# Optimization experiments

Measured on AMD Instinct MI355X. Metric: run time of the kernel, lower is better.

Reference implementation:

```python
import jax, jax.numpy as jnp
import numpy as np

DIM = 1024
HEADS = 16
HEAD_DIM = DIM // HEADS
MAX_SEQ = 4096
BATCH = 16
POSITION = MAX_SEQ - 1


def setup_inputs() -> dict:
    key = jax.random.key(0)
    ks = jax.random.split(key, 8)
    s = 0.02  # weight init scale, typical for transformer linears
    return {
        "token": jax.random.normal(ks[0], (BATCH, 1, DIM), dtype=jnp.float32),
        "k_cache": jax.random.normal(ks[1], (BATCH, MAX_SEQ, HEADS, HEAD_DIM), dtype=jnp.float32),
        "v_cache": jax.random.normal(ks[2], (BATCH, MAX_SEQ, HEADS, HEAD_DIM), dtype=jnp.float32),
        "Wq": jax.random.normal(ks[3], (DIM, DIM), dtype=jnp.float32) * s,
        "Wk": jax.random.normal(ks[4], (DIM, DIM), dtype=jnp.float32) * s,
        "Wv": jax.random.normal(ks[5], (DIM, DIM), dtype=jnp.float32) * s,
        "Wo": jax.random.normal(ks[6], (DIM, DIM), dtype=jnp.float32) * s,
        "position": POSITION,
    }


def reference(token, k_cache, v_cache, Wq, Wk, Wv, Wo, position):
    # Decode step: single-query attention against KV cache (FlexDecodingModule.decode).
    B = token.shape[0]
    # QKV projections (torch Linear: x @ W.T), bias=False
    q = (token @ Wq.T).reshape(B, 1, HEADS, HEAD_DIM)
    k = (token @ Wk.T).reshape(B, 1, HEADS, HEAD_DIM)
    v = (token @ Wv.T).reshape(B, 1, HEADS, HEAD_DIM)
    # Inline KV-cache append at `position` (static python int)
    kc = k_cache.at[:, position].set(k[:, 0])
    vc = v_cache.at[:, position].set(v[:, 0])
    past_k = kc[:, : position + 1]  # [B, L, H, D]
    past_v = vc[:, : position + 1]
    # Causal score_mod with offset=position, q_idx=0 => all kv_idx<=position visible (no mask)
    scale = 1.0 / np.sqrt(HEAD_DIM).astype(np.float32)
    scores = jnp.einsum("bqhd,bkhd->bhqk", q, past_k) * scale  # [B, H, 1, L]
    attn = jax.nn.softmax(scores, axis=-1)
    out = jnp.einsum("bhqk,bkhd->bqhd", attn, past_v)  # [B, 1, H, D]
    out = out.reshape(B, 1, DIM)
    return out @ Wo.T
```

## Files before the change

### kernel.cpp

```cpp
#include <hip/hip_runtime.h>
#include <hip/hip_bf16.h>
#include <math.h>

#define DIM 1024
#define HEADS 16
#define HEAD_DIM 64
#define MAXSEQ 4096
#define BATCH 16
#define SEQ_PER_BLK 32
#define NBLK (MAXSEQ / SEQ_PER_BLK)
#define NTILES (SEQ_PER_BLK / 4)

typedef float v4f __attribute__((ext_vector_type(4)));

__device__ __forceinline__ void gl16(v4f& dst, const float* p) {
  asm volatile("global_load_dwordx4 %0, %1, off" : "=v"(dst) : "v"(p)
               : "memory");
}

#define TILE_WAIT8(K, V)                                                     \
  asm volatile("s_waitcnt vmcnt(8)"                                          \
               : "+v"(K[0]), "+v"(K[1]), "+v"(K[2]), "+v"(K[3]),             \
                 "+v"(V[0]), "+v"(V[1]), "+v"(V[2]), "+v"(V[3])::"memory")
#define TILE_WAIT0(K, V)                                                     \
  asm volatile("s_waitcnt vmcnt(0)"                                          \
               : "+v"(K[0]), "+v"(K[1]), "+v"(K[2]), "+v"(K[3]),             \
                 "+v"(V[0]), "+v"(V[1]), "+v"(V[2]), "+v"(V[3])::"memory")

__global__ __launch_bounds__(256) void qkv_proj(
    const float* __restrict__ token,
    const float* __restrict__ Wq, const float* __restrict__ Wk,
    const float* __restrict__ Wv,
    float* __restrict__ out ) {
  __shared__ float tok[BATCH * DIM];
  for (int idx = threadIdx.x; idx < BATCH * DIM; idx += 256)
    tok[idx] = token[idx];
  __syncthreads();

  const float* W = (blockIdx.y == 0) ? Wq : ((blockIdx.y == 1) ? Wk : Wv);
  float* o = out + (size_t)blockIdx.y * BATCH * DIM;

  const int wave = threadIdx.x >> 6;
  const int lane = threadIdx.x & 63;
  const int i0 = blockIdx.x * 16 + wave * 4;

  float acc[4][16];
#pragma unroll
  for (int ii = 0; ii < 4; ++ii)
#pragma unroll
    for (int b = 0; b < 16; ++b) acc[ii][b] = 0.f;

  for (int t = 0; t < 16; ++t) {
    const int j = t * 64 + lane;
    float tk[16];
#pragma unroll
    for (int b = 0; b < 16; ++b) tk[b] = tok[b * DIM + j];
#pragma unroll
    for (int ii = 0; ii < 4; ++ii) {
      const float w = W[(size_t)(i0 + ii) * DIM + j];
#pragma unroll
      for (int b = 0; b < 16; ++b) acc[ii][b] = fmaf(w, tk[b], acc[ii][b]);
    }
  }

#pragma unroll
  for (int ii = 0; ii < 4; ++ii)
#pragma unroll
    for (int b = 0; b < 16; ++b) {
      float v = acc[ii][b];
#pragma unroll
      for (int m = 32; m >= 1; m >>= 1) v += __shfl_xor(v, m);
      if (lane == 0) o[(size_t)b * DIM + i0 + ii] = v;
    }
}

__global__ __launch_bounds__(256, 4) void attn_partial(
    const float* __restrict__ kc, const float* __restrict__ vc,
    const float* __restrict__ qkv, const int* __restrict__ pos_p,
    float* __restrict__ part) {
  const int blk = blockIdx.x, b = blockIdx.y;
  const int t = threadIdx.x;
  const int h = t >> 4, lq = t & 15;
  const int pos = pos_p[0];
  const int s0 = blk * SEQ_PER_BLK;

  const float scale = 0.125f;
  v4f q4 = *(const v4f*)(qkv + (size_t)b * DIM + 4 * t);
  q4 *= scale;
  __builtin_amdgcn_sched_barrier(0);

  const float* kp = kc + (size_t)b * MAXSEQ * DIM + (size_t)s0 * DIM + 4 * t;
  const float* vp = vc + (size_t)b * MAXSEQ * DIM + (size_t)s0 * DIM + 4 * t;

  v4f kb[2][4], vb[2][4];

  auto stage = [&](int buf) {
#pragma unroll
    for (int r = 0; r < 4; ++r) {
      gl16(kb[buf][r], kp); kp += DIM;
      gl16(vb[buf][r], vp); vp += DIM;
    }
  };

  float m = -INFINITY, lsum = 0.f;
  v4f a4 = {0.f, 0.f, 0.f, 0.f};

  auto compute = [&](int buf, int srow) {
    float sc[4];
#pragma unroll
    for (int r = 0; r < 4; ++r) {
      const v4f k4 = kb[buf][r];
      sc[r] = q4.x * k4.x + q4.y * k4.y + q4.z * k4.z + q4.w * k4.w;
    }
#pragma unroll
    for (int r = 0; r < 4; ++r) {
      sc[r] += __shfl_xor(sc[r], 1);
      sc[r] += __shfl_xor(sc[r], 2);
      sc[r] += __shfl_xor(sc[r], 4);
      sc[r] += __shfl_xor(sc[r], 8);
    }
#pragma unroll
    for (int r = 0; r < 4; ++r)
      if (srow + r >= pos) sc[r] = -INFINITY;

    const float tm = fmaxf(fmaxf(sc[0], sc[1]), fmaxf(sc[2], sc[3]));
    const float m_new = fmaxf(m, tm);
    const float corr = (m_new == -INFINITY) ? 1.f : __expf(m - m_new);
    lsum *= corr;
    a4 *= corr;
    m = m_new;
#pragma unroll
    for (int r = 0; r < 4; ++r) {
      const float pp = (sc[r] == -INFINITY) ? 0.f : __expf(sc[r] - m);
      lsum += pp;
      a4 += vb[buf][r] * pp;
    }
  };

  stage(0);
#pragma unroll
  for (int tt = 0; tt < NTILES - 1; ++tt) {
    stage((tt + 1) & 1);
    TILE_WAIT8(kb[tt & 1], vb[tt & 1]);
    __builtin_amdgcn_sched_barrier(0);
    compute(tt & 1, s0 + tt * 4);
  }
  TILE_WAIT0(kb[(NTILES - 1) & 1], vb[(NTILES - 1) & 1]);
  __builtin_amdgcn_sched_barrier(0);
  compute((NTILES - 1) & 1, s0 + (NTILES - 1) * 4);

  const size_t base = (((size_t)(b * HEADS + h)) * NBLK + blk) * 66;
  part[base + 2 + lq * 4 + 0] = a4.x;
  part[base + 2 + lq * 4 + 1] = a4.y;
  part[base + 2 + lq * 4 + 2] = a4.z;
  part[base + 2 + lq * 4 + 3] = a4.w;
  if (lq == 0) { part[base] = m; part[base + 1] = lsum; }
}

__global__ __launch_bounds__(256) void attn_combine(
    const float* __restrict__ part, const float* __restrict__ qkv,
    float* __restrict__ attn) {
  const int bh = blockIdx.x;
  const int b = bh >> 4, hh = bh & 15;
  const int g = threadIdx.x >> 6, d = threadIdx.x & 63;
  const float* p0 = part + (size_t)bh * NBLK * 66;

  const float qd = qkv[(size_t)b * DIM + hh * HEAD_DIM + d];
  const float kd = qkv[(size_t)BATCH * DIM + (size_t)b * DIM + hh * HEAD_DIM + d];
  const float vd = qkv[2 * (size_t)BATCH * DIM + (size_t)b * DIM + hh * HEAD_DIM + d];

  float sn = qd * kd;
  sn += __shfl_xor(sn, 1);
  sn += __shfl_xor(sn, 2);
  sn += __shfl_xor(sn, 4);
  sn += __shfl_xor(sn, 8);
  sn += __shfl_xor(sn, 16);
  sn += __shfl_xor(sn, 32);
  sn *= 0.125f;

  float M = sn;
  for (int c = g; c < NBLK; c += 4) M = fmaxf(M, p0[c * 66]);

  __shared__ float sM[4], sL[4], sO[4][64];
  if (d == 0) sM[g] = M;
  __syncthreads();
  M = fmaxf(fmaxf(sM[0], sM[1]), fmaxf(sM[2], sM[3]));

  float L = 0.f, o = 0.f;
  if (g == 0) {
    const float wn = __expf(sn - M);
    L = wn;
    o = wn * vd;
  }
  for (int c = g; c < NBLK; c += 4) {
    const float mc = p0[c * 66];
    if (mc > -INFINITY) {
      const float w = __expf(mc - M);
      L += p0[c * 66 + 1] * w;
      o = fmaf(p0[c * 66 + 2 + d], w, o);
    }
  }
  sO[g][d] = o;
  if (d == 0) sL[g] = L;
  __syncthreads();
  if (g == 0) {
    o = sO[0][d] + sO[1][d] + sO[2][d] + sO[3][d];
    L = sL[0] + sL[1] + sL[2] + sL[3];
    attn[(size_t)b * DIM + hh * HEAD_DIM + d] = o / L;
  }
}

__global__ __launch_bounds__(256) void o_proj(
    const float* __restrict__ attn, const float* __restrict__ Wo,
    float* __restrict__ out) {
  __shared__ float tok[BATCH * DIM];
  for (int idx = threadIdx.x; idx < BATCH * DIM; idx += 256)
    tok[idx] = attn[idx];
  __syncthreads();

  const int wave = threadIdx.x >> 6;
  const int lane = threadIdx.x & 63;
  const int i0 = blockIdx.x * 16 + wave * 4;

  float acc[4][16];
#pragma unroll
  for (int ii = 0; ii < 4; ++ii)
#pragma unroll
    for (int b = 0; b < 16; ++b) acc[ii][b] = 0.f;

  for (int t = 0; t < 16; ++t) {
    const int j = t * 64 + lane;
    float tk[16];
#pragma unroll
    for (int b = 0; b < 16; ++b) tk[b] = tok[b * DIM + j];
#pragma unroll
    for (int ii = 0; ii < 4; ++ii) {
      const float w = Wo[(size_t)(i0 + ii) * DIM + j];
#pragma unroll
      for (int b = 0; b < 16; ++b) acc[ii][b] = fmaf(w, tk[b], acc[ii][b]);
    }
  }

#pragma unroll
  for (int ii = 0; ii < 4; ++ii)
#pragma unroll
    for (int b = 0; b < 16; ++b) {
      float v = acc[ii][b];
#pragma unroll
      for (int m = 32; m >= 1; m >>= 1) v += __shfl_xor(v, m);
      if (lane == 0) out[(size_t)b * DIM + i0 + ii] = v;
    }
}

extern "C" void kernel_launch(void* const* d_in, const int* in_sizes, int n_in,
                              void* d_out, int out_size, void* d_ws, size_t ws_size,
                              hipStream_t stream) {
  const float* token = (const float*)d_in[0];
  const float* kc = (const float*)d_in[1];
  const float* vc = (const float*)d_in[2];
  const float* Wq = (const float*)d_in[3];
  const float* Wk = (const float*)d_in[4];
  const float* Wv = (const float*)d_in[5];
  const float* Wo = (const float*)d_in[6];
  const int* pos = (const int*)d_in[7];
  float* out = (float*)d_out;
  float* ws = (float*)d_ws;

  float* qkv = ws;
  float* part = ws + 3 * BATCH * DIM;
  float* attn = part + (size_t)BATCH * HEADS * NBLK * 66;

  hipLaunchKernelGGL(qkv_proj, dim3(64, 3), dim3(256), 0, stream,
                     token, Wq, Wk, Wv, qkv);
  hipLaunchKernelGGL(attn_partial, dim3(NBLK, BATCH), dim3(256), 0,
                     stream, kc, vc, qkv, pos, part);
  hipLaunchKernelGGL(attn_combine, dim3(BATCH * HEADS), dim3(256), 0, stream,
                     part, qkv, attn);
  hipLaunchKernelGGL(o_proj, dim3(64), dim3(256), 0, stream, attn, Wo, out);
  (void)in_sizes; (void)n_in; (void)out_size; (void)ws_size;
}
```

Baseline: 198.2 us.

## Remap attention partial so each wave streams full rows over its own sequence range

Reorganizes attn_partial so each wave owns a contiguous chunk of sequence rows and loads a whole 4KB row per step, with each lane holding four heads. Previously the 256 threads of a block split one row. Blocks drop from 128 to 32 per batch and each block yields four wave-level partials, so the combine kernel now reduces 128 partials per head. The change aims to lengthen per-wave streaming runs, cut the grid count and keep two rows in flight per wave. In exchange it uses more registers (occupancy hint lowered from 4 to 2 blocks) and launches fewer total blocks, which can reduce how many loads are outstanding at once across the GPU.

```diff
diff --git a/kernel.cpp b/kernel.cpp
--- a/kernel.cpp
+++ b/kernel.cpp
@@ -7,9 +7,10 @@
 #define HEAD_DIM 64
 #define MAXSEQ 4096
 #define BATCH 16
-#define SEQ_PER_BLK 32
-#define NBLK (MAXSEQ / SEQ_PER_BLK)
-#define NTILES (SEQ_PER_BLK / 4)
+#define NBLKS 32
+#define ROWS_PER_BLK (MAXSEQ / NBLKS)
+#define ROWS_PER_WAVE (ROWS_PER_BLK / 4)
+#define NPART (NBLKS * 4)
 
 typedef float v4f __attribute__((ext_vector_type(4)));
 
@@ -18,11 +19,11 @@
                : "memory");
 }
 
-#define TILE_WAIT8(K, V)                                                     \
+#define ROW_WAIT8(K, V)                                                      \
   asm volatile("s_waitcnt vmcnt(8)"                                          \
                : "+v"(K[0]), "+v"(K[1]), "+v"(K[2]), "+v"(K[3]),             \
                  "+v"(V[0]), "+v"(V[1]), "+v"(V[2]), "+v"(V[3])::"memory")
-#define TILE_WAIT0(K, V)                                                     \
+#define ROW_WAIT0(K, V)                                                      \
   asm volatile("s_waitcnt vmcnt(0)"                                          \
                : "+v"(K[0]), "+v"(K[1]), "+v"(K[2]), "+v"(K[3]),             \
                  "+v"(V[0]), "+v"(V[1]), "+v"(V[2]), "+v"(V[3])::"memory")
@@ -74,87 +75,111 @@
     }
 }
 
-__global__ __launch_bounds__(256, 4) void attn_partial(
+__global__ __launch_bounds__(256, 2) void attn_partial(
     const float* __restrict__ kc, const float* __restrict__ vc,
     const float* __restrict__ qkv, const int* __restrict__ pos_p,
     float* __restrict__ part) {
   const int blk = blockIdx.x, b = blockIdx.y;
   const int t = threadIdx.x;
-  const int h = t >> 4, lq = t & 15;
+  const int w = t >> 6, lane = t & 63;
+  const int g = lane >> 4, lq = lane & 15;
   const int pos = pos_p[0];
-  const int s0 = blk * SEQ_PER_BLK;
+  const int srow0 = blk * ROWS_PER_BLK + w * ROWS_PER_WAVE;
 
   const float scale = 0.125f;
-  v4f q4 = *(const v4f*)(qkv + (size_t)b * DIM + 4 * t);
-  q4 *= scale;
+  v4f q4[4];
+#pragma unroll
+  for (int i = 0; i < 4; ++i) {
+    q4[i] = *(const v4f*)(qkv + (size_t)b * DIM + (4 * i + g) * HEAD_DIM +
+                          lq * 4);
+    q4[i] *= scale;
+  }
   __builtin_amdgcn_sched_barrier(0);
 
-  const float* kp = kc + (size_t)b * MAXSEQ * DIM + (size_t)s0 * DIM + 4 * t;
-  const float* vp = vc + (size_t)b * MAXSEQ * DIM + (size_t)s0 * DIM + 4 * t;
-
-  v4f kb[2][4], vb[2][4];
-
-  auto stage = [&](int buf) {
-#pragma unroll
-    for (int r = 0; r < 4; ++r) {
-      gl16(kb[buf][r], kp); kp += DIM;
-      gl16(vb[buf][r], vp); vp += DIM;
+  const float* kp = kc + (size_t)b * MAXSEQ * DIM + (size_t)srow0 * DIM +
+                    lane * 4;
+  const float* vp = vc + (size_t)b * MAXSEQ * DIM + (size_t)srow0 * DIM +
+                    lane * 4;
+
+  v4f k0[4], v0[4], k1[4], v1[4];
+
+#define STAGE(K, V, r)                                                       \
+  {                                                                          \
+    const float* kr = kp + (size_t)(r)*DIM;                                  \
+    const float* vr = vp + (size_t)(r)*DIM;                                  \
+    gl16(K[0], kr); gl16(K[1], kr + 256);                                    \
+    gl16(K[2], kr + 512); gl16(K[3], kr + 768);                              \
+    gl16(V[0], vr); gl16(V[1], vr + 256);                                    \
+    gl16(V[2], vr + 512); gl16(V[3], vr + 768);                              \
+  }
+
+  float m[4], lsum[4];
+  v4f acc[4];
+#pragma unroll
+  for (int i = 0; i < 4; ++i) {
+    m[i] = -INFINITY;
+    lsum[i] = 0.f;
+    acc[i] = (v4f){0.f, 0.f, 0.f, 0.f};
+  }
+
+  auto compute = [&](const v4f (&K)[4], const v4f (&V)[4], int r) {
+    const int s = srow0 + r;
+    if (s >= pos) return;
+    float sc[4];
+#pragma unroll
+    for (int i = 0; i < 4; ++i)
+      sc[i] = q4[i].x * K[i].x + q4[i].y * K[i].y + q4[i].z * K[i].z +
+              q4[i].w * K[i].w;
+#pragma unroll
+    for (int i = 0; i < 4; ++i) {
+      sc[i] += __shfl_xor(sc[i], 1);
+      sc[i] += __shfl_xor(sc[i], 2);
+      sc[i] += __shfl_xor(sc[i], 4);
+      sc[i] += __shfl_xor(sc[i], 8);
+    }
+#pragma unroll
+    for (int i = 0; i < 4; ++i) {
+      const float mn = fmaxf(m[i], sc[i]);
+      const float corr = __expf(m[i] - mn);
+      const float p = __expf(sc[i] - mn);
+      lsum[i] = lsum[i] * corr + p;
+      acc[i] = acc[i] * corr + V[i] * p;
+      m[i] = mn;
     }
   };
 
-  float m = -INFINITY, lsum = 0.f;
-  v4f a4 = {0.f, 0.f, 0.f, 0.f};
-
-  auto compute = [&](int buf, int srow) {
-    float sc[4];
-#pragma unroll
-    for (int r = 0; r < 4; ++r) {
-      const v4f k4 = kb[buf][r];
-      sc[r] = q4.x * k4.x + q4.y * k4.y + q4.z * k4.z + q4.w * k4.w;
-    }
-#pragma unroll
-    for (int r = 0; r < 4; ++r) {
-      sc[r] += __shfl_xor(sc[r], 1);
-      sc[r] += __shfl_xor(sc[r], 2);
-      sc[r] += __shfl_xor(sc[r], 4);
-      sc[r] += __shfl_xor(sc[r], 8);
-    }
-#pragma unroll
-    for (int r = 0; r < 4; ++r)
-      if (srow + r >= pos) sc[r] = -INFINITY;
-
-    const float tm = fmaxf(fmaxf(sc[0], sc[1]), fmaxf(sc[2], sc[3]));
-    const float m_new = fmaxf(m, tm);
-    const float corr = (m_new == -INFINITY) ? 1.f : __expf(m - m_new);
-    lsum *= corr;
-    a4 *= corr;
-    m = m_new;
-#pragma unroll
-    for (int r = 0; r < 4; ++r) {
-      const float pp = (sc[r] == -INFINITY) ? 0.f : __expf(sc[r] - m);
-      lsum += pp;
-      a4 += vb[buf][r] * pp;
-    }
-  };
-
-  stage(0);
-#pragma unroll
-  for (int tt = 0; tt < NTILES - 1; ++tt) {
-    stage((tt + 1) & 1);
-    TILE_WAIT8(kb[tt & 1], vb[tt & 1]);
+  STAGE(k0, v0, 0);
+  STAGE(k1, v1, 1);
+#pragma unroll 1
+  for (int r = 0; r <= ROWS_PER_WAVE - 4; r += 2) {
+    ROW_WAIT8(k0, v0);
     __builtin_amdgcn_sched_barrier(0);
-    compute(tt & 1, s0 + tt * 4);
-  }
-  TILE_WAIT0(kb[(NTILES - 1) & 1], vb[(NTILES - 1) & 1]);
+    compute(k0, v0, r);
+    STAGE(k0, v0, r + 2);
+    ROW_WAIT8(k1, v1);
+    __builtin_amdgcn_sched_barrier(0);
+    compute(k1, v1, r + 1);
+    STAGE(k1, v1, r + 3);
+  }
+  ROW_WAIT8(k0, v0);
   __builtin_amdgcn_sched_barrier(0);
-  compute((NTILES - 1) & 1, s0 + (NTILES - 1) * 4);
-
-  const size_t base = (((size_t)(b * HEADS + h)) * NBLK + blk) * 66;
-  part[base + 2 + lq * 4 + 0] = a4.x;
-  part[base + 2 + lq * 4 + 1] = a4.y;
-  part[base + 2 + lq * 4 + 2] = a4.z;
-  part[base + 2 + lq * 4 + 3] = a4.w;
-  if (lq == 0) { part[base] = m; part[base + 1] = lsum; }
+  compute(k0, v0, ROWS_PER_WAVE - 2);
+  ROW_WAIT0(k1, v1);
+  __builtin_amdgcn_sched_barrier(0);
+  compute(k1, v1, ROWS_PER_WAVE - 1);
+#undef STAGE
+
+  const int pblk = blk * 4 + w;
+#pragma unroll
+  for (int i = 0; i < 4; ++i) {
+    const int head = 4 * i + g;
+    const size_t base = (((size_t)(b * HEADS + head)) * NPART + pblk) * 66;
+    part[base + 2 + lq * 4 + 0] = acc[i].x;
+    part[base + 2 + lq * 4 + 1] = acc[i].y;
+    part[base + 2 + lq * 4 + 2] = acc[i].z;
+    part[base + 2 + lq * 4 + 3] = acc[i].w;
+    if (lq == 0) { part[base] = m[i]; part[base + 1] = lsum[i]; }
+  }
 }
 
 __global__ __launch_bounds__(256) void attn_combine(
@@ -162,8 +187,8 @@
     float* __restrict__ attn) {
   const int bh = blockIdx.x;
   const int b = bh >> 4, hh = bh & 15;
-  const int g = threadIdx.x >> 6, d = threadIdx.x & 63;
-  const float* p0 = part + (size_t)bh * NBLK * 66;
+  const int gr = threadIdx.x >> 6, d = threadIdx.x & 63;
+  const float* p0 = part + (size_t)bh * NPART * 66;
 
   const float qd = qkv[(size_t)b * DIM + hh * HEAD_DIM + d];
   const float kd = qkv[(size_t)BATCH * DIM + (size_t)b * DIM + hh * HEAD_DIM + d];
@@ -179,20 +204,20 @@
   sn *= 0.125f;
 
   float M = sn;
-  for (int c = g; c < NBLK; c += 4) M = fmaxf(M, p0[c * 66]);
+  for (int c = gr; c < NPART; c += 4) M = fmaxf(M, p0[c * 66]);
 
   __shared__ float sM[4], sL[4], sO[4][64];
-  if (d == 0) sM[g] = M;
+  if (d == 0) sM[gr] = M;
   __syncthreads();
   M = fmaxf(fmaxf(sM[0], sM[1]), fmaxf(sM[2], sM[3]));
 
   float L = 0.f, o = 0.f;
-  if (g == 0) {
+  if (gr == 0) {
     const float wn = __expf(sn - M);
     L = wn;
     o = wn * vd;
   }
-  for (int c = g; c < NBLK; c += 4) {
+  for (int c = gr; c < NPART; c += 4) {
     const float mc = p0[c * 66];
     if (mc > -INFINITY) {
       const float w = __expf(mc - M);
@@ -200,10 +225,10 @@
       o = fmaf(p0[c * 66 + 2 + d], w, o);
     }
   }
-  sO[g][d] = o;
-  if (d == 0) sL[g] = L;
+  sO[gr][d] = o;
+  if (d == 0) sL[gr] = L;
   __syncthreads();
-  if (g == 0) {
+  if (gr == 0) {
     o = sO[0][d] + sO[1][d] + sO[2][d] + sO[3][d];
     L = sL[0] + sL[1] + sL[2] + sL[3];
     attn[(size_t)b * DIM + hh * HEAD_DIM + d] = o / L;
@@ -268,11 +293,11 @@
 
   float* qkv = ws;
   float* part = ws + 3 * BATCH * DIM;
-  float* attn = part + (size_t)BATCH * HEADS * NBLK * 66;
+  float* attn = part + (size_t)BATCH * HEADS * NPART * 66;
 
   hipLaunchKernelGGL(qkv_proj, dim3(64, 3), dim3(256), 0, stream,
                      token, Wq, Wk, Wv, qkv);
-  hipLaunchKernelGGL(attn_partial, dim3(NBLK, BATCH), dim3(256), 0,
+  hipLaunchKernelGGL(attn_partial, dim3(NBLKS, BATCH), dim3(256), 0,
                      stream, kc, vc, qkv, pos, part);
   hipLaunchKernelGGL(attn_combine, dim3(BATCH * HEADS), dim3(256), 0, stream,
                      part, qkv, attn);
```

Measured after the change: 174.5 us. 1.14x faster.
